# Kernel tuning notes

Measured on AMD Instinct MI355X. Metric: run time of the kernel, lower is better.

Reference implementation:

```python
import jax, jax.numpy as jnp
import numpy as np
from jax import lax

B, M, N = 4096, 306, 984
LAMBDA = 0.1
MAX_ITER = 50


def setup_inputs() -> dict:
    key = jax.random.key(0)
    k1, k2, k3, k4 = jax.random.split(key, 4)
    return {
        "r_real": jax.random.normal(k1, (B, M), dtype=jnp.float32),
        "r_imag": jax.random.normal(k2, (B, M), dtype=jnp.float32),
        # phi buffer: torch.randn(M, N, dtype=complex64) -> real/imag each ~N(0, 1/2)?
        # torch.randn(complex64) draws real & imag each from N(0, 1/sqrt(2)^2)=N(0,0.5).
        "phi_real": jax.random.normal(k3, (M, N), dtype=jnp.float32) * np.float32(1.0 / np.sqrt(2.0)),
        "phi_imag": jax.random.normal(k4, (M, N), dtype=jnp.float32) * np.float32(1.0 / np.sqrt(2.0)),
    }


def reference(r_real, r_imag, phi_real, phi_imag):
    phi = (phi_real + 1j * phi_imag).astype(jnp.complex64)          # [M, N]
    r = (r_real + 1j * r_imag).astype(jnp.complex64)                # [B, M]
    # step_size = 1 / ||phi||_2^2  (spectral norm squared)
    step = (1.0 / jnp.linalg.norm(phi, ord=2) ** 2).real.astype(jnp.float32)
    thresh = (LAMBDA * step).astype(jnp.float32)
    phi_c = jnp.conj(phi)

    def body(w, _):
        # error = w @ phi.T - r : [B, M]
        error = jnp.einsum("bn,mn->bm", w, phi) - r
        # gradient = error @ conj(phi) : [B, N]
        grad = jnp.einsum("bm,mn->bn", error, phi_c)
        w_next = w - step * grad
        w_mag = jnp.abs(w_next)
        new_mag = jax.nn.relu(w_mag - thresh)
        # polar(new_mag, angle(w_next))
        w_new = (new_mag * jnp.exp(1j * jnp.angle(w_next))).astype(jnp.complex64)
        return w_new, None

    w0 = jnp.zeros((r.shape[0], N), dtype=jnp.complex64)
    w, _ = lax.scan(body, w0, None, length=MAX_ITER)
    return jnp.abs(w).astype(jnp.float32)
```

## Files before the change

kernel.cpp:

```cpp
#include <hip/hip_runtime.h>
#include <math.h>

#define Bb 4096
#define Mm 306
#define Nn 984
#define NCP 1024
#define KA 2048
#define ITERS 50
#define KSQ 9

typedef _Float16 f16x8 __attribute__((ext_vector_type(8)));
typedef float f32x16 __attribute__((ext_vector_type(16)));

__device__ __forceinline__ void cmac(float2& c, const float2 a, const float2 b) {
    c.x = fmaf(a.x, b.x, c.x);
    c.x = fmaf(-a.y, b.y, c.x);
    c.y = fmaf(a.x, b.y, c.y);
    c.y = fmaf(a.y, b.x, c.y);
}

__device__ __forceinline__ unsigned short f16bits(float v) {
    union { _Float16 h; unsigned short u; } cv;
    cv.h = (_Float16)v;
    return cv.u;
}
__device__ __forceinline__ float f16lo(unsigned int u) {
    union { unsigned short s; _Float16 h; } cv; cv.s = (unsigned short)(u & 0xffffu);
    return (float)cv.h;
}
__device__ __forceinline__ float f16hi(unsigned int u) {
    union { unsigned short s; _Float16 h; } cv; cv.s = (unsigned short)(u >> 16);
    return (float)cv.h;
}

__device__ __forceinline__ void load_lds16(const void* g, void* l) {
    __builtin_amdgcn_global_load_lds((const __attribute__((address_space(1))) void*)g,
                                     (__attribute__((address_space(3))) void*)l, 16, 0, 0);
}

__device__ __forceinline__ size_t swzA(int b, int c) {
    return ((size_t)(((b >> 7) * 32 + (c >> 5)) * 1024 + ((c >> 2) & 7) * 128 + (b & 127))) * 4 + (c & 3);
}
__device__ __forceinline__ size_t swzB(int jr, int q) {
    return ((size_t)(((jr >> 7) * 32 + (q >> 5)) * 1024 + ((q >> 2) & 7) * 128 + (jr & 127))) * 4 + (q & 3);
}
__device__ __forceinline__ size_t swzA2(int b, int c) {
    return ((size_t)(((b >> 7) * 10 + (c >> 5)) * 1024 + ((c >> 2) & 7) * 128 + (b & 127))) * 4 + (c & 3);
}
__device__ __forceinline__ size_t swzB2(int jr, int q) {
    return ((size_t)(((jr >> 7) * 10 + (q >> 5)) * 1024 + ((q >> 2) & 7) * 128 + (jr & 127))) * 4 + (q & 3);
}

__global__ void gram_kernel(const float* __restrict__ pr, const float* __restrict__ pi,
                            float2* __restrict__ G) {
    __shared__ float2 As[32][33];
    __shared__ float2 Bs[32][33];
    int tx = threadIdx.x, ty = threadIdx.y;
    int t = ty * 16 + tx;
    int i0 = blockIdx.y * 32, j0 = blockIdx.x * 32;
    int zs = blockIdx.z * 246;
    int ze = zs + 246 < Nn ? zs + 246 : Nn;
    float2 acc[2][2] = {};
    for (int k0 = zs; k0 < ze; k0 += 32) {
        #pragma unroll
        for (int rep = 0; rep < 4; ++rep) {
            int idx = t + rep * 256;
            int rr = idx >> 5, cc = idx & 31;
            int gk = k0 + cc;
            int gi = i0 + rr, gj = j0 + rr;
            float2 a = make_float2(0.f, 0.f), b = make_float2(0.f, 0.f);
            if (gk < ze) {
                if (gi < Mm) a = make_float2(pr[(size_t)gi * Nn + gk], pi[(size_t)gi * Nn + gk]);
                if (gj < Mm) b = make_float2(pr[(size_t)gj * Nn + gk], pi[(size_t)gj * Nn + gk]);
            }
            As[rr][cc] = a; Bs[rr][cc] = b;
        }
        __syncthreads();
        #pragma unroll 8
        for (int kk = 0; kk < 32; ++kk) {
            float2 a0 = As[ty * 2][kk], a1 = As[ty * 2 + 1][kk];
            float2 b0 = Bs[tx * 2][kk], b1 = Bs[tx * 2 + 1][kk];
            #define GMAC(qq, aa, bb) \
                qq.x = fmaf(aa.x, bb.x, qq.x); qq.x = fmaf(aa.y, bb.y, qq.x); \
                qq.y = fmaf(aa.y, bb.x, qq.y); qq.y = fmaf(-aa.x, bb.y, qq.y);
            GMAC(acc[0][0], a0, b0) GMAC(acc[0][1], a0, b1)
            GMAC(acc[1][0], a1, b0) GMAC(acc[1][1], a1, b1)
            #undef GMAC
        }
        __syncthreads();
    }
    #pragma unroll
    for (int i = 0; i < 2; ++i) {
        int gi = i0 + ty * 2 + i;
        #pragma unroll
        for (int j = 0; j < 2; ++j) {
            int gj = j0 + tx * 2 + j;
            if (gi < Mm && gj < Mm) {
                atomicAdd(&G[gi * Mm + gj].x, acc[i][j].x);
                atomicAdd(&G[gi * Mm + gj].y, acc[i][j].y);
            }
        }
    }
}

__global__ void frob_kernel(const float2* __restrict__ H, float* __restrict__ slot, int n) {
    int idx = blockIdx.x * blockDim.x + threadIdx.x;
    int stride = gridDim.x * blockDim.x;
    float s = 0.f;
    for (int i = idx; i < n; i += stride) {
        float2 v = H[i];
        s = fmaf(v.x, v.x, s);
        s = fmaf(v.y, v.y, s);
    }
    #pragma unroll
    for (int o = 32; o > 0; o >>= 1) s += __shfl_down(s, o, 64);
    __shared__ float wsum[4];
    int lane = threadIdx.x & 63, wv = threadIdx.x >> 6;
    if (lane == 0) wsum[wv] = s;
    __syncthreads();
    if (threadIdx.x == 0) atomicAdd(slot, wsum[0] + wsum[1] + wsum[2] + wsum[3]);
}

__global__ void sqmm_kernel(const float2* __restrict__ A, float2* __restrict__ C,
                            const float* __restrict__ fslot) {
    __shared__ float2 As[32][33];
    __shared__ float2 Bs[32][33];
    float inv = 1.0f / fslot[0];
    int tx = threadIdx.x, ty = threadIdx.y;
    int t = ty * 16 + tx;
    int r0 = blockIdx.y * 32, c0 = blockIdx.x * 32;
    int zs = blockIdx.z * 80;
    int ze = zs + 80 < Mm ? zs + 80 : Mm;
    float2 acc[2][2] = {};
    for (int k0 = zs; k0 < ze; k0 += 32) {
        #pragma unroll
        for (int i = 0; i < 4; ++i) {
            int idx = t + i * 256;
            int rr = idx >> 5, cc = idx & 31;
            int gr = r0 + rr, gk = k0 + cc;
            As[rr][cc] = (gr < Mm && gk < ze) ? A[gr * Mm + gk] : make_float2(0.f, 0.f);
            int gk2 = k0 + rr, gc = c0 + cc;
            Bs[rr][cc] = (gk2 < ze && gc < Mm) ? A[gk2 * Mm + gc] : make_float2(0.f, 0.f);
        }
        __syncthreads();
        #pragma unroll 8
        for (int kk = 0; kk < 32; ++kk) {
            float2 a0 = As[ty * 2][kk], a1 = As[ty * 2 + 1][kk];
            float2 b0 = Bs[kk][tx * 2], b1 = Bs[kk][tx * 2 + 1];
            cmac(acc[0][0], a0, b0); cmac(acc[0][1], a0, b1);
            cmac(acc[1][0], a1, b0); cmac(acc[1][1], a1, b1);
        }
        __syncthreads();
    }
    #pragma unroll
    for (int i = 0; i < 2; ++i) {
        int gr = r0 + ty * 2 + i;
        #pragma unroll
        for (int j = 0; j < 2; ++j) {
            int gc = c0 + tx * 2 + j;
            if (gr < Mm && gc < Mm) {
                atomicAdd(&C[gr * Mm + gc].x, acc[i][j].x * inv);
                atomicAdd(&C[gr * Mm + gc].y, acc[i][j].y * inv);
            }
        }
    }
}

__global__ void rayleigh_kernel(const float2* __restrict__ H, const float2* __restrict__ G,
                                float* __restrict__ sc) {
    __shared__ float2 v[Mm];
    __shared__ float rn[320], rd[320];
    int t = threadIdx.x;
    if (t < Mm) {
        float2 s = make_float2(0.f, 0.f);
        for (int j = 0; j < Mm; ++j) { float2 h = H[t * Mm + j]; s.x += h.x; s.y += h.y; }
        v[t] = s;
    }
    __syncthreads();
    float num = 0.f, den = 0.f;
    if (t < Mm) {
        float2 u = make_float2(0.f, 0.f);
        for (int k = 0; k < Mm; ++k) {
            float2 g = G[k * Mm + t];
            float2 vk = v[k];
            u.x = fmaf(g.x, vk.x, u.x); u.x = fmaf(g.y, vk.y, u.x);
            u.y = fmaf(g.x, vk.y, u.y); u.y = fmaf(-g.y, vk.x, u.y);
        }
        float2 vt = v[t];
        num = vt.x * u.x + vt.y * u.y;
        den = vt.x * vt.x + vt.y * vt.y;
    }
    rn[t] = num; rd[t] = den;
    __syncthreads();
    if (t == 0) {
        float sn = 0.f, sd = 0.f;
        for (int i = 0; i < 320; ++i) { sn += rn[i]; sd += rd[i]; }
        float lam = sn / sd;
        float step = 1.0f / lam;
        sc[0] = step;
        sc[1] = 0.1f * step;
    }
}

__global__ void qpack_kernel(const float* __restrict__ pr, const float* __restrict__ pi,
                             unsigned int* __restrict__ Bu, const float* __restrict__ sc) {
    __shared__ float Pnr[16][33], Pni[16][33];
    __shared__ float Pcr[16][33], Pci[16][33];
    float nstep = -sc[0];
    int t = threadIdx.x;
    int tx = t & 15, ty = t >> 4;
    int n0 = blockIdx.x * 32, c0 = blockIdx.y * 32;
    float2 q[2][2] = {};
    for (int m0 = 0; m0 < Mm; m0 += 16) {
        #pragma unroll
        for (int rep = 0; rep < 2; ++rep) {
            int idx = t + rep * 256;
            int mm = idx >> 5, col = idx & 31;
            int gm = m0 + mm;
            float2 a = make_float2(0.f, 0.f), b = make_float2(0.f, 0.f);
            if (gm < Mm) {
                if (n0 + col < Nn) a = make_float2(pr[(size_t)gm * Nn + n0 + col], pi[(size_t)gm * Nn + n0 + col]);
                if (c0 + col < Nn) b = make_float2(pr[(size_t)gm * Nn + c0 + col], pi[(size_t)gm * Nn + c0 + col]);
            }
            Pnr[mm][col] = a.x; Pni[mm][col] = a.y;
            Pcr[mm][col] = b.x; Pci[mm][col] = b.y;
        }
        __syncthreads();
        #pragma unroll
        for (int mm = 0; mm < 16; ++mm) {
            float2 a0 = make_float2(Pnr[mm][ty * 2], Pni[mm][ty * 2]);
            float2 a1 = make_float2(Pnr[mm][ty * 2 + 1], Pni[mm][ty * 2 + 1]);
            float2 b0 = make_float2(Pcr[mm][tx * 2], Pci[mm][tx * 2]);
            float2 b1 = make_float2(Pcr[mm][tx * 2 + 1], Pci[mm][tx * 2 + 1]);
            #define QMAC(qq, aa, bb) \
                qq.x = fmaf(aa.x, bb.x, qq.x); qq.x = fmaf(aa.y, bb.y, qq.x); \
                qq.y = fmaf(aa.y, bb.x, qq.y); qq.y = fmaf(-aa.x, bb.y, qq.y);
            QMAC(q[0][0], a0, b0) QMAC(q[0][1], a0, b1)
            QMAC(q[1][0], a1, b0) QMAC(q[1][1], a1, b1)
            #undef QMAC
        }
        __syncthreads();
    }
    #pragma unroll
    for (int i = 0; i < 2; ++i) {
        int n = n0 + ty * 2 + i;
        #pragma unroll
        for (int j = 0; j < 2; ++j) {
            int c = c0 + tx * 2 + j;
            if (n < Nn && c < Nn) {
                float MR = fmaf(nstep, q[i][j].x, (n == c) ? 1.0f : 0.0f);
                float MI = nstep * q[i][j].y;
                unsigned short hR = f16bits(MR);
                unsigned short hI = f16bits(MI);
                unsigned short nhI = hI ^ 0x8000u;
                int jr = ((c >> 5) * 64) + (c & 31);
                Bu[swzB(jr, n)]      = (unsigned)hR | ((unsigned)nhI << 16);
                Bu[swzB(jr + 32, n)] = (unsigned)hI | ((unsigned)hR << 16);
            }
        }
    }
}

__global__ void rpack_kernel(const float* __restrict__ rr, const float* __restrict__ ri,
                             unsigned int* __restrict__ rp16) {
    int b = blockIdx.x * 256 + threadIdx.x;
    int m = blockIdx.y;
    rp16[swzA2(b, m)] = (unsigned)f16bits(rr[(size_t)b * Mm + m]) |
                        ((unsigned)f16bits(ri[(size_t)b * Mm + m]) << 16);
}

__global__ void ppack2_kernel(const float* __restrict__ pr, const float* __restrict__ pi,
                              unsigned int* __restrict__ B2u, const float* __restrict__ sc) {
    int n = blockIdx.x * 256 + threadIdx.x;
    int m = blockIdx.y;
    if (n >= Nn) return;
    float s = sc[0];
    float xr = pr[(size_t)m * Nn + n], xi = pi[(size_t)m * Nn + n];
    unsigned short x = f16bits(-s * xr), y = f16bits(-s * xi);
    int jr2 = ((n >> 5) * 64) + (n & 31);
    B2u[swzB2(jr2, m)]      = (unsigned)x | ((unsigned)y << 16);
    B2u[swzB2(jr2 + 32, m)] = (unsigned)(y ^ 0x8000u) | ((unsigned)x << 16);
}

__global__ __launch_bounds__(256, 2) void rphi_mfma_kernel(
    const _Float16* __restrict__ rp16, const _Float16* __restrict__ B2,
    unsigned int* __restrict__ rph16) {
    __shared__ _Float16 As[8192];
    __shared__ _Float16 Bs[8192];
    int tid = threadIdx.x;
    int lane = tid & 63, wv = tid >> 6;
    int wm = wv & 1, wn = wv >> 1;
    int bblk = blockIdx.x, nblk = blockIdx.y;
    int l31 = lane & 31, lh = lane >> 5;

    f32x16 acc[2][2] = {};

    for (int kt = 0; kt < 10; ++kt) {
        #pragma unroll
        for (int c = 0; c < 4; ++c) {
            int u = c * 256 + tid;
            const char* ga = (const char*)rp16 + (((size_t)(bblk * 10 + kt)) * 1024 + u) * 16;
            load_lds16(ga, &As[(size_t)(c * 256 + wv * 64) * 8]);
            const char* gb = (const char*)B2 + (((size_t)(nblk * 10 + kt)) * 1024 + u) * 16;
            load_lds16(gb, &Bs[(size_t)(c * 256 + wv * 64) * 8]);
        }
        __syncthreads();
        #pragma unroll
        for (int s = 0; s < 4; ++s) {
            int kq = s * 2 + lh;
            f16x8 af[2], bfr[2];
            #pragma unroll
            for (int mt = 0; mt < 2; ++mt)
                af[mt] = *reinterpret_cast<const f16x8*>(
                    &As[(size_t)(kq * 128 + wm * 64 + mt * 32 + l31) * 8]);
            #pragma unroll
            for (int nt = 0; nt < 2; ++nt)
                bfr[nt] = *reinterpret_cast<const f16x8*>(
                    &Bs[(size_t)(kq * 128 + wn * 64 + nt * 32 + l31) * 8]);
            #pragma unroll
            for (int mt = 0; mt < 2; ++mt)
                #pragma unroll
                for (int nt = 0; nt < 2; ++nt)
                    acc[mt][nt] = __builtin_amdgcn_mfma_f32_32x32x16_f16(af[mt], bfr[nt], acc[mt][nt], 0, 0, 0);
        }
        __syncthreads();
    }

    int b0 = bblk * 128;
    int c = nblk * 64 + wn * 32 + l31;
    #pragma unroll
    for (int mt = 0; mt < 2; ++mt) {
        #pragma unroll
        for (int reg = 0; reg < 16; ++reg) {
            int row = b0 + wm * 64 + mt * 32 + ((reg & 3) + 8 * (reg >> 2) + 4 * lh);
            rph16[(size_t)row * NCP + c] =
                (unsigned)f16bits(-acc[mt][0][reg]) | ((unsigned)f16bits(-acc[mt][1][reg]) << 16);
        }
    }
}

__global__ __launch_bounds__(256, 2) void ista7_kernel(
    const _Float16* __restrict__ wfi, const _Float16* __restrict__ Bq,
    unsigned int* __restrict__ wfo,
    const unsigned int* __restrict__ rph16,
    const float* __restrict__ sc, float* __restrict__ out, int last) {
    __shared__ _Float16 As[8192];
    __shared__ _Float16 Bs[8192];
    int tid = threadIdx.x;
    int lane = tid & 63, wv = tid >> 6;
    int wm = wv & 1, wn = wv >> 1;
    int id = blockIdx.x;
    int bblk = id >> 4;
    int nblk = id & 15;
    int l31 = lane & 31, lh = lane >> 5;

    f32x16 acc[2][2] = {};

    for (int kt = 0; kt < 32; ++kt) {
        #pragma unroll
        for (int c = 0; c < 4; ++c) {
            int u = c * 256 + tid;
            const char* ga = (const char*)wfi + (((size_t)(bblk * 32 + kt)) * 1024 + u) * 16;
            load_lds16(ga, &As[(size_t)(c * 256 + wv * 64) * 8]);
            const char* gb = (const char*)Bq + (((size_t)(nblk * 32 + kt)) * 1024 + u) * 16;
            load_lds16(gb, &Bs[(size_t)(c * 256 + wv * 64) * 8]);
        }
        __syncthreads();
        #pragma unroll
        for (int s = 0; s < 4; ++s) {
            int kq = s * 2 + lh;
            f16x8 af[2], bfr[2];
            #pragma unroll
            for (int mt = 0; mt < 2; ++mt)
                af[mt] = *reinterpret_cast<const f16x8*>(
                    &As[(size_t)(kq * 128 + wm * 64 + mt * 32 + l31) * 8]);
            #pragma unroll
            for (int nt = 0; nt < 2; ++nt)
                bfr[nt] = *reinterpret_cast<const f16x8*>(
                    &Bs[(size_t)(kq * 128 + wn * 64 + nt * 32 + l31) * 8]);
            #pragma unroll
            for (int mt = 0; mt < 2; ++mt)
                #pragma unroll
                for (int nt = 0; nt < 2; ++nt)
                    acc[mt][nt] = __builtin_amdgcn_mfma_f32_32x32x16_f16(af[mt], bfr[nt], acc[mt][nt], 0, 0, 0);
        }
        __syncthreads();
    }

    float thr = sc[1];
    int b0 = bblk * 128;
    int c = nblk * 64 + wn * 32 + l31;
    #pragma unroll
    for (int mt = 0; mt < 2; ++mt) {
        #pragma unroll
        for (int reg = 0; reg < 16; ++reg) {
            int row = b0 + wm * 64 + mt * 32 + ((reg & 3) + 8 * (reg >> 2) + 4 * lh);
            unsigned int ru = rph16[(size_t)row * NCP + c];
            float zr = acc[mt][0][reg] + f16lo(ru);
            float zi = acc[mt][1][reg] + f16hi(ru);
            float mag = sqrtf(zr * zr + zi * zi);
            float nm = mag - thr;
            float f = (nm > 0.f) ? (nm / mag) : 0.f;
            wfo[swzA(row, c)] = (unsigned)f16bits(zr * f) | ((unsigned)f16bits(zi * f) << 16);
            if (last && c < Nn) out[(size_t)row * Nn + c] = fmaxf(nm, 0.f);
        }
    }
}

extern "C" void kernel_launch(void* const* d_in, const int* in_sizes, int n_in,
                              void* d_out, int out_size, void* d_ws, size_t ws_size,
                              hipStream_t stream) {
    const float* rr = (const float*)d_in[0];
    const float* ri = (const float*)d_in[1];
    const float* pr = (const float*)d_in[2];
    const float* pi = (const float*)d_in[3];
    float* out = (float*)d_out;

    char* ws = (char*)d_ws;
    size_t off = 0;
    _Float16* wf0 = (_Float16*)(ws + off); off += (size_t)Bb * KA * sizeof(_Float16);
    _Float16* wf1 = (_Float16*)(ws + off); off += (size_t)Bb * KA * sizeof(_Float16);
    _Float16* Bq  = (_Float16*)(ws + off); off += (size_t)2048 * 2048 * sizeof(_Float16);
    unsigned int* rph16 = (unsigned int*)(ws + off); off += (size_t)Bb * NCP * 4;
    _Float16* rp16 = (_Float16*)(ws + off); off += (size_t)Bb * 640 * sizeof(_Float16);
    _Float16* B2  = (_Float16*)(ws + off); off += (size_t)2048 * 640 * sizeof(_Float16);
    float2* G = (float2*)(ws + off);     off += (size_t)Mm * Mm * sizeof(float2);
    float2* H1 = (float2*)(ws + off);    off += (size_t)Mm * Mm * sizeof(float2);
    float2* H2 = (float2*)(ws + off);    off += (size_t)Mm * Mm * sizeof(float2);
    float* slots = (float*)(ws + off);   off += 64 * sizeof(float);
    float* sc = slots + 32;

    (void)hipMemsetAsync(wf0, 0, (size_t)Bb * KA * sizeof(_Float16), stream);
    (void)hipMemsetAsync(Bq, 0, (size_t)2048 * 2048 * sizeof(_Float16), stream);
    (void)hipMemsetAsync(rp16, 0, (size_t)Bb * 640 * sizeof(_Float16), stream);
    (void)hipMemsetAsync(B2, 0, (size_t)2048 * 640 * sizeof(_Float16), stream);
    (void)hipMemsetAsync(slots, 0, 64 * sizeof(float), stream);
    (void)hipMemsetAsync(G, 0, (size_t)Mm * Mm * sizeof(float2), stream);

    gram_kernel<<<dim3(10, 10, 4), dim3(16, 16), 0, stream>>>(pr, pi, G);
    float2* bufs[2] = { H1, H2 };
    const float2* src = G;
    for (int s = 0; s < KSQ; ++s) {
        frob_kernel<<<128, 256, 0, stream>>>(src, slots + s, Mm * Mm);
        float2* dst = bufs[s & 1];
        (void)hipMemsetAsync(dst, 0, (size_t)Mm * Mm * sizeof(float2), stream);
        sqmm_kernel<<<dim3(10, 10, 4), dim3(16, 16), 0, stream>>>(src, dst, slots + s);
        src = dst;
    }
    rayleigh_kernel<<<1, 320, 0, stream>>>(src, G, sc);

    qpack_kernel<<<dim3(31, 31), 256, 0, stream>>>(pr, pi, (unsigned int*)Bq, sc);
    rpack_kernel<<<dim3(16, Mm), 256, 0, stream>>>(rr, ri, (unsigned int*)rp16);
    ppack2_kernel<<<dim3(4, Mm), 256, 0, stream>>>(pr, pi, (unsigned int*)B2, sc);
    rphi_mfma_kernel<<<dim3(32, 16), 256, 0, stream>>>(rp16, B2, rph16);

    _Float16* wbuf[2] = { wf0, wf1 };
    for (int it = 0; it < ITERS; ++it) {
        ista7_kernel<<<512, 256, 0, stream>>>(
            wbuf[it & 1], Bq, (unsigned int*)wbuf[(it + 1) & 1], rph16, sc, out,
            it == ITERS - 1 ? 1 : 0);
    }
}
```

Measured before the change: 3.006 ms.

## Double-buffer LDS tiles in MFMA GEMM kernels to overlap loads with compute

The rphi and ista7 MFMA kernels now use two LDS buffers. Each K-tile's global-to-LDS loads are issued while the previous tile is multiplied, using vmcnt waits and raw barriers instead of a full sync after every load. This is meant to hide global memory latency in the per-iteration ISTA GEMM. In exchange, LDS per block doubles, and the last loop step prefetches one tile past the block's K range, which is never used and may read out of bounds. qpack also switches its shared arrays to float2 pairs.

```diff
diff --git a/kernel.cpp b/kernel.cpp
--- a/kernel.cpp
+++ b/kernel.cpp
@@ -49,6 +49,38 @@
 }
 __device__ __forceinline__ size_t swzB2(int jr, int q) {
     return ((size_t)(((jr >> 7) * 10 + (q >> 5)) * 1024 + ((q >> 2) & 7) * 128 + (jr & 127))) * 4 + (q & 3);
+}
+
+__device__ __forceinline__ void stage_tile(const char* gA, const char* gB, int kt,
+                                           _Float16* Ad, _Float16* Bd, int tid, int wv) {
+    #pragma unroll
+    for (int c = 0; c < 4; ++c) {
+        int u = c * 256 + tid;
+        load_lds16(gA + ((size_t)kt * 1024 + u) * 16, &Ad[(size_t)(c * 256 + wv * 64) * 8]);
+        load_lds16(gB + ((size_t)kt * 1024 + u) * 16, &Bd[(size_t)(c * 256 + wv * 64) * 8]);
+    }
+}
+
+__device__ __forceinline__ void compute_tile(const _Float16* Asrc, const _Float16* Bsrc,
+                                             f32x16 acc[2][2], int wm, int wn, int l31, int lh) {
+    #pragma unroll
+    for (int s = 0; s < 4; ++s) {
+        int kq = s * 2 + lh;
+        f16x8 af[2], bf[2];
+        #pragma unroll
+        for (int mt = 0; mt < 2; ++mt)
+            af[mt] = *reinterpret_cast<const f16x8*>(
+                &Asrc[(size_t)(kq * 128 + wm * 64 + mt * 32 + l31) * 8]);
+        #pragma unroll
+        for (int nt = 0; nt < 2; ++nt)
+            bf[nt] = *reinterpret_cast<const f16x8*>(
+                &Bsrc[(size_t)(kq * 128 + wn * 64 + nt * 32 + l31) * 8]);
+        #pragma unroll
+        for (int mt = 0; mt < 2; ++mt)
+            #pragma unroll
+            for (int nt = 0; nt < 2; ++nt)
+                acc[mt][nt] = __builtin_amdgcn_mfma_f32_32x32x16_f16(af[mt], bf[nt], acc[mt][nt], 0, 0, 0);
+    }
 }
 
 __global__ void gram_kernel(const float* __restrict__ pr, const float* __restrict__ pi,
@@ -204,8 +236,8 @@
 
 __global__ void qpack_kernel(const float* __restrict__ pr, const float* __restrict__ pi,
                              unsigned int* __restrict__ Bu, const float* __restrict__ sc) {
-    __shared__ float Pnr[16][33], Pni[16][33];
-    __shared__ float Pcr[16][33], Pci[16][33];
+    __shared__ float2 Pn[16][33];
+    __shared__ float2 Pc[16][33];
     float nstep = -sc[0];
     int t = threadIdx.x;
     int tx = t & 15, ty = t >> 4;
@@ -222,16 +254,13 @@
                 if (n0 + col < Nn) a = make_float2(pr[(size_t)gm * Nn + n0 + col], pi[(size_t)gm * Nn + n0 + col]);
                 if (c0 + col < Nn) b = make_float2(pr[(size_t)gm * Nn + c0 + col], pi[(size_t)gm * Nn + c0 + col]);
             }
-            Pnr[mm][col] = a.x; Pni[mm][col] = a.y;
-            Pcr[mm][col] = b.x; Pci[mm][col] = b.y;
+            Pn[mm][col] = a; Pc[mm][col] = b;
         }
         __syncthreads();
         #pragma unroll
         for (int mm = 0; mm < 16; ++mm) {
-            float2 a0 = make_float2(Pnr[mm][ty * 2], Pni[mm][ty * 2]);
-            float2 a1 = make_float2(Pnr[mm][ty * 2 + 1], Pni[mm][ty * 2 + 1]);
-            float2 b0 = make_float2(Pcr[mm][tx * 2], Pci[mm][tx * 2]);
-            float2 b1 = make_float2(Pcr[mm][tx * 2 + 1], Pci[mm][tx * 2 + 1]);
+            float2 a0 = Pn[mm][ty * 2], a1 = Pn[mm][ty * 2 + 1];
+            float2 b0 = Pc[mm][tx * 2], b1 = Pc[mm][tx * 2 + 1];
             #define QMAC(qq, aa, bb) \
                 qq.x = fmaf(aa.x, bb.x, qq.x); qq.x = fmaf(aa.y, bb.y, qq.x); \
                 qq.y = fmaf(aa.y, bb.x, qq.y); qq.y = fmaf(-aa.x, bb.y, qq.y);
@@ -285,8 +314,8 @@
 __global__ __launch_bounds__(256, 2) void rphi_mfma_kernel(
     const _Float16* __restrict__ rp16, const _Float16* __restrict__ B2,
     unsigned int* __restrict__ rph16) {
-    __shared__ _Float16 As[8192];
-    __shared__ _Float16 Bs[8192];
+    __shared__ _Float16 As0[8192], Bs0[8192];
+    __shared__ _Float16 As1[8192], Bs1[8192];
     int tid = threadIdx.x;
     int lane = tid & 63, wv = tid >> 6;
     int wm = wv & 1, wn = wv >> 1;
@@ -295,35 +324,21 @@
 
     f32x16 acc[2][2] = {};
 
-    for (int kt = 0; kt < 10; ++kt) {
-        #pragma unroll
-        for (int c = 0; c < 4; ++c) {
-            int u = c * 256 + tid;
-            const char* ga = (const char*)rp16 + (((size_t)(bblk * 10 + kt)) * 1024 + u) * 16;
-            load_lds16(ga, &As[(size_t)(c * 256 + wv * 64) * 8]);
-            const char* gb = (const char*)B2 + (((size_t)(nblk * 10 + kt)) * 1024 + u) * 16;
-            load_lds16(gb, &Bs[(size_t)(c * 256 + wv * 64) * 8]);
-        }
-        __syncthreads();
-        #pragma unroll
-        for (int s = 0; s < 4; ++s) {
-            int kq = s * 2 + lh;
-            f16x8 af[2], bfr[2];
-            #pragma unroll
-            for (int mt = 0; mt < 2; ++mt)
-                af[mt] = *reinterpret_cast<const f16x8*>(
-                    &As[(size_t)(kq * 128 + wm * 64 + mt * 32 + l31) * 8]);
-            #pragma unroll
-            for (int nt = 0; nt < 2; ++nt)
-                bfr[nt] = *reinterpret_cast<const f16x8*>(
-                    &Bs[(size_t)(kq * 128 + wn * 64 + nt * 32 + l31) * 8]);
-            #pragma unroll
-            for (int mt = 0; mt < 2; ++mt)
-                #pragma unroll
-                for (int nt = 0; nt < 2; ++nt)
-                    acc[mt][nt] = __builtin_amdgcn_mfma_f32_32x32x16_f16(af[mt], bfr[nt], acc[mt][nt], 0, 0, 0);
-        }
-        __syncthreads();
+    const char* gA = (const char*)rp16 + (size_t)bblk * 10 * 1024 * 16;
+    const char* gB = (const char*)B2 + (size_t)nblk * 10 * 1024 * 16;
+
+    stage_tile(gA, gB, 0, As0, Bs0, tid, wv);
+    for (int kt = 0; kt < 10; kt += 2) {
+        stage_tile(gA, gB, kt + 1, As1, Bs1, tid, wv);
+        asm volatile("s_waitcnt vmcnt(8)" ::: "memory");
+        __builtin_amdgcn_s_barrier();
+        compute_tile(As0, Bs0, acc, wm, wn, l31, lh);
+        __builtin_amdgcn_s_barrier();
+        stage_tile(gA, gB, kt + 2, As0, Bs0, tid, wv);
+        asm volatile("s_waitcnt vmcnt(8)" ::: "memory");
+        __builtin_amdgcn_s_barrier();
+        compute_tile(As1, Bs1, acc, wm, wn, l31, lh);
+        __builtin_amdgcn_s_barrier();
     }
 
     int b0 = bblk * 128;
@@ -344,8 +359,8 @@
     unsigned int* __restrict__ wfo,
     const unsigned int* __restrict__ rph16,
     const float* __restrict__ sc, float* __restrict__ out, int last) {
-    __shared__ _Float16 As[8192];
-    __shared__ _Float16 Bs[8192];
+    __shared__ _Float16 As0[8192], Bs0[8192];
+    __shared__ _Float16 As1[8192], Bs1[8192];
     int tid = threadIdx.x;
     int lane = tid & 63, wv = tid >> 6;
     int wm = wv & 1, wn = wv >> 1;
@@ -356,35 +371,21 @@
 
     f32x16 acc[2][2] = {};
 
-    for (int kt = 0; kt < 32; ++kt) {
-        #pragma unroll
-        for (int c = 0; c < 4; ++c) {
-            int u = c * 256 + tid;
-            const char* ga = (const char*)wfi + (((size_t)(bblk * 32 + kt)) * 1024 + u) * 16;
-            load_lds16(ga, &As[(size_t)(c * 256 + wv * 64) * 8]);
-            const char* gb = (const char*)Bq + (((size_t)(nblk * 32 + kt)) * 1024 + u) * 16;
-            load_lds16(gb, &Bs[(size_t)(c * 256 + wv * 64) * 8]);
-        }
-        __syncthreads();
-        #pragma unroll
-        for (int s = 0; s < 4; ++s) {
-            int kq = s * 2 + lh;
-            f16x8 af[2], bfr[2];
-            #pragma unroll
-            for (int mt = 0; mt < 2; ++mt)
-                af[mt] = *reinterpret_cast<const f16x8*>(
-                    &As[(size_t)(kq * 128 + wm * 64 + mt * 32 + l31) * 8]);
-            #pragma unroll
-            for (int nt = 0; nt < 2; ++nt)
-                bfr[nt] = *reinterpret_cast<const f16x8*>(
-                    &Bs[(size_t)(kq * 128 + wn * 64 + nt * 32 + l31) * 8]);
-            #pragma unroll
-            for (int mt = 0; mt < 2; ++mt)
-                #pragma unroll
-                for (int nt = 0; nt < 2; ++nt)
-                    acc[mt][nt] = __builtin_amdgcn_mfma_f32_32x32x16_f16(af[mt], bfr[nt], acc[mt][nt], 0, 0, 0);
-        }
-        __syncthreads();
+    const char* gA = (const char*)wfi + (size_t)bblk * 32 * 1024 * 16;
+    const char* gB = (const char*)Bq + (size_t)nblk * 32 * 1024 * 16;
+
+    stage_tile(gA, gB, 0, As0, Bs0, tid, wv);
+    for (int kt = 0; kt < 32; kt += 2) {
+        stage_tile(gA, gB, kt + 1, As1, Bs1, tid, wv);
+        asm volatile("s_waitcnt vmcnt(8)" ::: "memory");
+        __builtin_amdgcn_s_barrier();
+        compute_tile(As0, Bs0, acc, wm, wn, l31, lh);
+        __builtin_amdgcn_s_barrier();
+        stage_tile(gA, gB, kt + 2, As0, Bs0, tid, wv);
+        asm volatile("s_waitcnt vmcnt(8)" ::: "memory");
+        __builtin_amdgcn_s_barrier();
+        compute_tile(As1, Bs1, acc, wm, wn, l31, lh);
+        __builtin_amdgcn_s_barrier();
     }
 
     float thr = sc[1];
```

New measurement: 3.048 ms. Within noise of the previous version (+1.4%).

## Double-buffer ISTA GEMM tiles and widen block to 128 columns

Applied to the files above, without the earlier changes.

The per-iteration ISTA kernel now computes a 128x128 output tile per block instead of 128x64, with half as many blocks. The K loop is software-pipelined: global-to-LDS loads for the next k-tile go into a second LDS buffer while the current one is consumed, with explicit vmcnt waits and raw barriers. The goal is to hide global-load latency and double the reuse of the A tile. In exchange it uses about 96KB of LDS and twice the accumulators, so occupancy is lower, and the last stage prefetches one unused tile past the end. qpack also stores phi in LDS as float2 rather than split real/imag arrays.

```diff
diff --git a/kernel.cpp b/kernel.cpp
--- a/kernel.cpp
+++ b/kernel.cpp
@@ -204,8 +204,8 @@
 
 __global__ void qpack_kernel(const float* __restrict__ pr, const float* __restrict__ pi,
                              unsigned int* __restrict__ Bu, const float* __restrict__ sc) {
-    __shared__ float Pnr[16][33], Pni[16][33];
-    __shared__ float Pcr[16][33], Pci[16][33];
+    __shared__ float2 Pn[16][33];
+    __shared__ float2 Pc[16][33];
     float nstep = -sc[0];
     int t = threadIdx.x;
     int tx = t & 15, ty = t >> 4;
@@ -222,16 +222,13 @@
                 if (n0 + col < Nn) a = make_float2(pr[(size_t)gm * Nn + n0 + col], pi[(size_t)gm * Nn + n0 + col]);
                 if (c0 + col < Nn) b = make_float2(pr[(size_t)gm * Nn + c0 + col], pi[(size_t)gm * Nn + c0 + col]);
             }
-            Pnr[mm][col] = a.x; Pni[mm][col] = a.y;
-            Pcr[mm][col] = b.x; Pci[mm][col] = b.y;
+            Pn[mm][col] = a; Pc[mm][col] = b;
         }
         __syncthreads();
         #pragma unroll
         for (int mm = 0; mm < 16; ++mm) {
-            float2 a0 = make_float2(Pnr[mm][ty * 2], Pni[mm][ty * 2]);
-            float2 a1 = make_float2(Pnr[mm][ty * 2 + 1], Pni[mm][ty * 2 + 1]);
-            float2 b0 = make_float2(Pcr[mm][tx * 2], Pci[mm][tx * 2]);
-            float2 b1 = make_float2(Pcr[mm][tx * 2 + 1], Pci[mm][tx * 2 + 1]);
+            float2 a0 = Pn[mm][ty * 2], a1 = Pn[mm][ty * 2 + 1];
+            float2 b0 = Pc[mm][tx * 2], b1 = Pc[mm][tx * 2 + 1];
             #define QMAC(qq, aa, bb) \
                 qq.x = fmaf(aa.x, bb.x, qq.x); qq.x = fmaf(aa.y, bb.y, qq.x); \
                 qq.y = fmaf(aa.y, bb.x, qq.y); qq.y = fmaf(-aa.x, bb.y, qq.y);
@@ -339,70 +336,104 @@
     }
 }
 
-__global__ __launch_bounds__(256, 2) void ista7_kernel(
+__global__ __launch_bounds__(256) void ista8_kernel(
     const _Float16* __restrict__ wfi, const _Float16* __restrict__ Bq,
     unsigned int* __restrict__ wfo,
     const unsigned int* __restrict__ rph16,
     const float* __restrict__ sc, float* __restrict__ out, int last) {
-    __shared__ _Float16 As[8192];
-    __shared__ _Float16 Bs[8192];
+    __shared__ _Float16 As0[8192], As1[8192];
+    __shared__ _Float16 Bs0[2][8192], Bs1[2][8192];
     int tid = threadIdx.x;
     int lane = tid & 63, wv = tid >> 6;
     int wm = wv & 1, wn = wv >> 1;
     int id = blockIdx.x;
-    int bblk = id >> 4;
-    int nblk = id & 15;
+    int bblk = id >> 3;
+    int nb2 = id & 7;
     int l31 = lane & 31, lh = lane >> 5;
 
-    f32x16 acc[2][2] = {};
-
-    for (int kt = 0; kt < 32; ++kt) {
-        #pragma unroll
-        for (int c = 0; c < 4; ++c) {
-            int u = c * 256 + tid;
-            const char* ga = (const char*)wfi + (((size_t)(bblk * 32 + kt)) * 1024 + u) * 16;
-            load_lds16(ga, &As[(size_t)(c * 256 + wv * 64) * 8]);
-            const char* gb = (const char*)Bq + (((size_t)(nblk * 32 + kt)) * 1024 + u) * 16;
-            load_lds16(gb, &Bs[(size_t)(c * 256 + wv * 64) * 8]);
-        }
-        __syncthreads();
-        #pragma unroll
-        for (int s = 0; s < 4; ++s) {
-            int kq = s * 2 + lh;
-            f16x8 af[2], bfr[2];
-            #pragma unroll
-            for (int mt = 0; mt < 2; ++mt)
-                af[mt] = *reinterpret_cast<const f16x8*>(
-                    &As[(size_t)(kq * 128 + wm * 64 + mt * 32 + l31) * 8]);
-            #pragma unroll
-            for (int nt = 0; nt < 2; ++nt)
-                bfr[nt] = *reinterpret_cast<const f16x8*>(
-                    &Bs[(size_t)(kq * 128 + wn * 64 + nt * 32 + l31) * 8]);
-            #pragma unroll
-            for (int mt = 0; mt < 2; ++mt)
-                #pragma unroll
-                for (int nt = 0; nt < 2; ++nt)
-                    acc[mt][nt] = __builtin_amdgcn_mfma_f32_32x32x16_f16(af[mt], bfr[nt], acc[mt][nt], 0, 0, 0);
-        }
-        __syncthreads();
-    }
+    f32x16 acc[2][2][2] = {};
+
+    const char* gA  = (const char*)wfi + (size_t)bblk * 32 * 1024 * 16;
+    const char* gB0 = (const char*)Bq + (size_t)(nb2 * 2 + 0) * 32 * 1024 * 16;
+    const char* gB1 = (const char*)Bq + (size_t)(nb2 * 2 + 1) * 32 * 1024 * 16;
+
+    #define STAGE8(kt, Ad, Bd)                                                        \
+        {                                                                             \
+            _Float16* Ap = (Ad);                                                      \
+            _Float16* Bp0 = &(Bd)[0][0];                                              \
+            _Float16* Bp1 = &(Bd)[1][0];                                              \
+            _Pragma("unroll")                                                         \
+            for (int cc = 0; cc < 4; ++cc) {                                          \
+                int u = cc * 256 + tid;                                               \
+                size_t ldst = (size_t)(cc * 256 + wv * 64) * 8;                       \
+                load_lds16(gA + ((size_t)(kt) * 1024 + u) * 16, &Ap[ldst]);           \
+                load_lds16(gB0 + ((size_t)(kt) * 1024 + u) * 16, &Bp0[ldst]);         \
+                load_lds16(gB1 + ((size_t)(kt) * 1024 + u) * 16, &Bp1[ldst]);         \
+            }                                                                         \
+        }
+
+    #define COMPUTE8(Asrc, Bsrc)                                                      \
+        {                                                                             \
+            _Pragma("unroll")                                                         \
+            for (int s = 0; s < 4; ++s) {                                             \
+                int kq = s * 2 + lh;                                                  \
+                f16x8 af[2], bf[2][2];                                                \
+                _Pragma("unroll")                                                     \
+                for (int mt = 0; mt < 2; ++mt)                                        \
+                    af[mt] = *reinterpret_cast<const f16x8*>(                         \
+                        &(Asrc)[(size_t)(kq * 128 + wm * 64 + mt * 32 + l31) * 8]);   \
+                _Pragma("unroll")                                                     \
+                for (int ct = 0; ct < 2; ++ct)                                        \
+                    _Pragma("unroll")                                                 \
+                    for (int nt = 0; nt < 2; ++nt)                                    \
+                        bf[ct][nt] = *reinterpret_cast<const f16x8*>(                 \
+                            &(Bsrc)[wn][(size_t)(kq * 128 + ct * 64 + nt * 32 + l31) * 8]); \
+                _Pragma("unroll")                                                     \
+                for (int mt = 0; mt < 2; ++mt)                                        \
+                    _Pragma("unroll")                                                 \
+                    for (int ct = 0; ct < 2; ++ct)                                    \
+                        _Pragma("unroll")                                             \
+                        for (int nt = 0; nt < 2; ++nt)                                \
+                            acc[mt][ct][nt] = __builtin_amdgcn_mfma_f32_32x32x16_f16( \
+                                af[mt], bf[ct][nt], acc[mt][ct][nt], 0, 0, 0);        \
+            }                                                                         \
+        }
+
+    STAGE8(0, As0, Bs0);
+    for (int kt = 0; kt < 32; kt += 2) {
+        STAGE8(kt + 1, As1, Bs1);
+        asm volatile("s_waitcnt vmcnt(12)" ::: "memory");
+        __builtin_amdgcn_s_barrier();
+        COMPUTE8(As0, Bs0);
+        __builtin_amdgcn_s_barrier();
+        STAGE8(kt + 2, As0, Bs0);
+        asm volatile("s_waitcnt vmcnt(12)" ::: "memory");
+        __builtin_amdgcn_s_barrier();
+        COMPUTE8(As1, Bs1);
+        __builtin_amdgcn_s_barrier();
+    }
+    #undef STAGE8
+    #undef COMPUTE8
 
     float thr = sc[1];
     int b0 = bblk * 128;
-    int c = nblk * 64 + wn * 32 + l31;
     #pragma unroll
     for (int mt = 0; mt < 2; ++mt) {
         #pragma unroll
-        for (int reg = 0; reg < 16; ++reg) {
-            int row = b0 + wm * 64 + mt * 32 + ((reg & 3) + 8 * (reg >> 2) + 4 * lh);
-            unsigned int ru = rph16[(size_t)row * NCP + c];
-            float zr = acc[mt][0][reg] + f16lo(ru);
-            float zi = acc[mt][1][reg] + f16hi(ru);
-            float mag = sqrtf(zr * zr + zi * zi);
-            float nm = mag - thr;
-            float f = (nm > 0.f) ? (nm / mag) : 0.f;
-            wfo[swzA(row, c)] = (unsigned)f16bits(zr * f) | ((unsigned)f16bits(zi * f) << 16);
-            if (last && c < Nn) out[(size_t)row * Nn + c] = fmaxf(nm, 0.f);
+        for (int ct = 0; ct < 2; ++ct) {
+            int c = nb2 * 128 + wn * 64 + ct * 32 + l31;
+            #pragma unroll
+            for (int reg = 0; reg < 16; ++reg) {
+                int row = b0 + wm * 64 + mt * 32 + ((reg & 3) + 8 * (reg >> 2) + 4 * lh);
+                unsigned int ru = rph16[(size_t)row * NCP + c];
+                float zr = acc[mt][ct][0][reg] + f16lo(ru);
+                float zi = acc[mt][ct][1][reg] + f16hi(ru);
+                float mag = sqrtf(zr * zr + zi * zi);
+                float nm = mag - thr;
+                float f = (nm > 0.f) ? (nm / mag) : 0.f;
+                wfo[swzA(row, c)] = (unsigned)f16bits(zr * f) | ((unsigned)f16bits(zi * f) << 16);
+                if (last && c < Nn) out[(size_t)row * Nn + c] = fmaxf(nm, 0.f);
+            }
         }
     }
 }
@@ -456,7 +487,7 @@
 
     _Float16* wbuf[2] = { wf0, wf1 };
     for (int it = 0; it < ITERS; ++it) {
-        ista7_kernel<<<512, 256, 0, stream>>>(
+        ista8_kernel<<<256, 256, 0, stream>>>(
             wbuf[it & 1], Bq, (unsigned int*)wbuf[(it + 1) & 1], rph16, sc, out,
             it == ITERS - 1 ? 1 : 0);
     }
```

New measurement: 3.676 ms. +22.3%, slower.
